# Performance work log

Hardware: AMD Instinct MI355X
Metric: run time of the kernel (lower is better)

The kernel has to match this reference:

```python
import jax, jax.numpy as jnp
import numpy as np

NF, D, H, HD, NL, FF = 5, 64, 8, 8, 2, 128   # features, d_model, heads, head_dim, layers, ffn
NQ, QL, NC = 8, 3, 3                          # qubits, quantum layers, classes


def pos_encoding(S, d):
    pos = np.arange(S, dtype=np.float32)[:, None]
    div = np.exp(np.arange(0, d, 2, dtype=np.float32) * (-np.log(10000.0) / d))
    pe = np.zeros((S, d), np.float32)
    pe[:, 0::2] = np.sin(pos * div)
    pe[:, 1::2] = np.cos(pos * div)
    return jnp.asarray(pe)


def layernorm(x, g, b, eps=1e-5):
    m = x.mean(-1, keepdims=True)
    v = ((x - m) ** 2).mean(-1, keepdims=True)
    return (x - m) * jax.lax.rsqrt(v + eps) * g + b


def apply1q(psi, U, w):
    # psi: (2,)*NQ complex state; apply 2x2 gate U on wire w
    p = jnp.moveaxis(psi, w, 0)
    sh = p.shape
    p = (U @ p.reshape(2, -1)).reshape(sh)
    return jnp.moveaxis(p, 0, w)


def cnot(psi, c, t):
    p = jnp.moveaxis(psi, (c, t), (0, 1))
    sh = p.shape
    p = p.reshape(2, 2, -1)
    p = jnp.stack([p[0], p[1, ::-1]], 0).reshape(sh)  # flip target when control=1
    return jnp.moveaxis(p, (0, 1), (c, t))


def rx_mat(t):
    c, s = jnp.cos(t / 2), jnp.sin(t / 2)
    return jnp.stack([jnp.stack([c + 0j, -1j * s]), jnp.stack([-1j * s, c + 0j])]).astype(jnp.complex64)


def rot_mat(phi, th, om):
    # qml.Rot = RZ(om) RY(th) RZ(phi)
    c, s = jnp.cos(th / 2), jnp.sin(th / 2)
    return jnp.stack([
        jnp.stack([jnp.exp(-0.5j * (phi + om)) * c, -jnp.exp(0.5j * (phi - om)) * s]),
        jnp.stack([jnp.exp(-0.5j * (phi - om)) * s, jnp.exp(0.5j * (phi + om)) * c]),
    ]).astype(jnp.complex64)


def quantum_circuit(angles, weights):
    # angles: [NQ], weights: [QL, NQ, 3]. Circuit: QL x (AngleEmbedding(RX) + StronglyEntanglingLayer(range=1))
    psi = jnp.zeros((2,) * NQ, jnp.complex64).at[(0,) * NQ].set(1.0)
    for l in range(QL):
        for w in range(NQ):
            psi = apply1q(psi, rx_mat(angles[w]), w)
        for w in range(NQ):
            psi = apply1q(psi, rot_mat(weights[l, w, 0], weights[l, w, 1], weights[l, w, 2]), w)
        for w in range(NQ):
            psi = cnot(psi, w, (w + 1) % NQ)
    prob = jnp.abs(psi) ** 2
    zs = []
    for w in range(NC):  # <Z_w> = p(0_w) - p(1_w)
        marg = prob.sum(axis=tuple(i for i in range(NQ) if i != w))
        zs.append(marg[0] - marg[1])
    # von Neumann entropy of wires 0..3 (trace out wires 4..7), natural log
    mat = psi.reshape(16, 16)
    rho = mat @ mat.conj().T
    ev = jnp.clip(jnp.linalg.eigvalsh(rho), 1e-10, 1.0)
    ent = -jnp.sum(ev * jnp.log(ev))
    return jnp.stack(zs), ent


def setup_inputs() -> dict:
    key = jax.random.key(0)
    ks = jax.random.split(key, 30)
    sc = 0.02
    inp = {
        'x': jax.random.normal(ks[0], (16, 1024, NF), jnp.float32),
        'Wemb': sc * jax.random.normal(ks[1], (NF, D)), 'bemb': jnp.zeros((D,)),
        'Wq': sc * jax.random.normal(ks[2], (NL, D, D)), 'bq': jnp.zeros((NL, D)),
        'Wk': sc * jax.random.normal(ks[3], (NL, D, D)), 'bk': jnp.zeros((NL, D)),
        'Wv': sc * jax.random.normal(ks[4], (NL, D, D)), 'bv': jnp.zeros((NL, D)),
        'Wo': sc * jax.random.normal(ks[5], (NL, D, D)), 'bo': jnp.zeros((NL, D)),
        'ln1g': jnp.ones((NL, D)), 'ln1b': jnp.zeros((NL, D)),
        'ln2g': jnp.ones((NL, D)), 'ln2b': jnp.zeros((NL, D)),
        'Wf1': sc * jax.random.normal(ks[6], (NL, D, FF)), 'bf1': jnp.zeros((NL, FF)),
        'Wf2': sc * jax.random.normal(ks[7], (NL, FF, D)), 'bf2': jnp.zeros((NL, D)),
        'Wp1': sc * jax.random.normal(ks[8], (D, 32)), 'bp1': jnp.zeros((32,)),
        'Wp2': sc * jax.random.normal(ks[9], (32, NQ)), 'bp2': jnp.zeros((NQ,)),
        'qweights': jax.random.normal(ks[10], (QL, NQ, 3)),
    }
    return inp


def reference(x, Wemb, bemb, Wq, bq, Wk, bk, Wv, bv, Wo, bo, ln1g, ln1b, ln2g, ln2b,
              Wf1, bf1, Wf2, bf2, Wp1, bp1, Wp2, bp2, qweights):
    B, S, _ = x.shape
    h = x @ Wemb + bemb + pos_encoding(S, D)[None]  # aug + dropout are identity in eval
    scale = np.float32(1.0 / np.sqrt(HD))
    for l in range(NL):
        q = (h @ Wq[l] + bq[l]).reshape(B, S, H, HD).transpose(0, 2, 1, 3)
        k = (h @ Wk[l] + bk[l]).reshape(B, S, H, HD).transpose(0, 2, 1, 3)
        v = (h @ Wv[l] + bv[l]).reshape(B, S, H, HD).transpose(0, 2, 1, 3)
        att = jax.nn.softmax(jnp.einsum('bhsd,bhtd->bhst', q, k) * scale, axis=-1)
        o = jnp.einsum('bhst,bhtd->bhsd', att, v).transpose(0, 2, 1, 3).reshape(B, S, D)
        h = layernorm(h + o @ Wo[l] + bo[l], ln1g[l], ln1b[l])
        ff = jax.nn.relu(h @ Wf1[l] + bf1[l]) @ Wf2[l] + bf2[l]
        h = layernorm(h + ff, ln2g[l], ln2b[l])
    pooled = h.mean(1)
    feats = jax.nn.relu(pooled @ Wp1 + bp1) @ Wp2 + bp2
    angles = jnp.tanh(feats) * np.float32(np.pi)
    logits, ent = jax.vmap(quantum_circuit, in_axes=(0, None))(angles, qweights)
    return logits, ent
```

## Files before the change

### kernel.cpp

```cpp
#include <hip/hip_runtime.h>
#include <math.h>

#define BB 16
#define SS 1024
#define NF 5
#define DD 64
#define HH 8
#define HDIM 8
#define NLAYER 2
#define FFD 128
#define NQ 8
#define QLAY 3
#define NC 3
#define NSWEEP 5
#define BHS_TOT (BB * HH * SS)

typedef __fp16 hf2 __attribute__((ext_vector_type(2)));
__device__ inline hf2 ash2(float f) { union { float f; hf2 h; } u; u.f = f; return u.h; }

__global__ __launch_bounds__(64) void k_embed(const float* __restrict__ x,
                                              const float* __restrict__ Wemb,
                                              const float* __restrict__ bemb,
                                              float* __restrict__ h) {
    int bs = blockIdx.x;
    int s  = bs & (SS - 1);
    int d  = threadIdx.x;
    const float* xr = x + bs * NF;
    float acc = bemb[d];
#pragma unroll
    for (int f = 0; f < NF; ++f) acc += xr[f] * Wemb[f * DD + d];
    int i = d >> 1;
    float div = expf((float)(2 * i) * (-9.210340371976184f / 64.0f));
    float ang = (float)s * div;
    float pe = (d & 1) ? cosf(ang) : sinf(ang);
    h[bs * DD + d] = acc + pe;
}

__global__ __launch_bounds__(64) void k_qkv(const float* __restrict__ h,
                                            const float* __restrict__ Wq, const float* __restrict__ bq,
                                            const float* __restrict__ Wk, const float* __restrict__ bk,
                                            const float* __restrict__ Wv, const float* __restrict__ bv,
                                            hf2* __restrict__ qh, hf2* __restrict__ kvh, int l) {
    __shared__ float hrow[4][DD];
    int d   = threadIdx.x;
    int bs0 = blockIdx.x * 4;
#pragma unroll
    for (int r = 0; r < 4; ++r) hrow[r][d] = h[(bs0 + r) * DD + d];
    __syncthreads();
    const float* wq = Wq + l * DD * DD;
    const float* wk = Wk + l * DD * DD;
    const float* wv = Wv + l * DD * DD;
    float aq[4], ak[4], av[4];
    float bqv = bq[l * DD + d], bkv = bk[l * DD + d], bvv = bv[l * DD + d];
#pragma unroll
    for (int r = 0; r < 4; ++r) { aq[r] = bqv; ak[r] = bkv; av[r] = bvv; }
#pragma unroll 4
    for (int i = 0; i < DD; ++i) {
        float wqv = wq[i * DD + d], wkv = wk[i * DD + d], wvv = wv[i * DD + d];
#pragma unroll
        for (int r = 0; r < 4; ++r) {
            float hv = hrow[r][i];
            aq[r] += hv * wqv; ak[r] += hv * wkv; av[r] += hv * wvv;
        }
    }
    int hh = d >> 3, hd = d & 7;
    const float qs = 0.3535533906f;
    float aqp[4], akp[4];
#pragma unroll
    for (int r = 0; r < 4; ++r) { aqp[r] = __shfl_xor(aq[r], 1); akp[r] = __shfl_xor(ak[r], 1); }
    if ((hd & 1) == 0) {
#pragma unroll
        for (int r = 0; r < 4; ++r) {
            int bs = bs0 + r;
            int b = bs >> 10, s = bs & 1023;
            int bh = b * HH + hh;
            int bhs = (bh << 10) | s;
            qh[bhs * 4 + (hd >> 1)] = __builtin_amdgcn_cvt_pkrtz(aq[r] * qs, aqp[r] * qs);
            int tp = s >> 1, par = s & 1;
            kvh[(bh * 512 + tp) * 16 + par * 4 + (hd >> 1)] =
                __builtin_amdgcn_cvt_pkrtz(ak[r], akp[r]);
        }
    }
#pragma unroll
    for (int r = 0; r < 4; r += 2) {
        int bs = bs0 + r;
        int b = bs >> 10, s = bs & 1023;
        int bh = b * HH + hh;
        int tp = s >> 1;
        kvh[(bh * 512 + tp) * 16 + 8 + hd] = __builtin_amdgcn_cvt_pkrtz(av[r], av[r + 1]);
    }
}

__global__ __launch_bounds__(256) void k_attn(const hf2* __restrict__ qh,
                                              const float4* __restrict__ kvh4,
                                              float* __restrict__ Apart,
                                              float* __restrict__ lpart,
                                              int nch) {
    __shared__ float4 KVs[1024];
    int bh  = blockIdx.x;
    int sg  = blockIdx.y & 3;
    int ch  = blockIdx.y >> 2;
    int tid = threadIdx.x;
    int s   = sg * 256 + tid;
    int tpc = 512 / nch;
    const float4* kp = kvh4 + (size_t)(bh * 512 + ch * tpc) * 4;
    for (int i = tid; i < tpc * 4; i += 256) KVs[i] = kp[i];
    float4 qv = ((const float4*)qh)[(bh << 10) | s];
    hf2 q01 = ash2(qv.x), q23 = ash2(qv.y), q45 = ash2(qv.z), q67 = ash2(qv.w);
    hf2 one2 = __builtin_amdgcn_cvt_pkrtz(1.f, 1.f);
    float ls = 0.f;
    float A[8] = {0,0,0,0,0,0,0,0};
    __syncthreads();
#pragma unroll 2
    for (int t = 0; t < tpc; ++t) {
        float4 f0 = KVs[4*t], f1 = KVs[4*t+1], f2 = KVs[4*t+2], f3 = KVs[4*t+3];
        float sc0 = __builtin_amdgcn_fdot2(q67, ash2(f0.w),
                    __builtin_amdgcn_fdot2(q45, ash2(f0.z),
                    __builtin_amdgcn_fdot2(q23, ash2(f0.y),
                    __builtin_amdgcn_fdot2(q01, ash2(f0.x), 0.f, false), false), false), false);
        float sc1 = __builtin_amdgcn_fdot2(q67, ash2(f1.w),
                    __builtin_amdgcn_fdot2(q45, ash2(f1.z),
                    __builtin_amdgcn_fdot2(q23, ash2(f1.y),
                    __builtin_amdgcn_fdot2(q01, ash2(f1.x), 0.f, false), false), false), false);
        float p0 = __expf(sc0), p1 = __expf(sc1);
        hf2 pp = __builtin_amdgcn_cvt_pkrtz(p0, p1);
        ls   = __builtin_amdgcn_fdot2(pp, one2,       ls,   false);
        A[0] = __builtin_amdgcn_fdot2(pp, ash2(f2.x), A[0], false);
        A[1] = __builtin_amdgcn_fdot2(pp, ash2(f2.y), A[1], false);
        A[2] = __builtin_amdgcn_fdot2(pp, ash2(f2.z), A[2], false);
        A[3] = __builtin_amdgcn_fdot2(pp, ash2(f2.w), A[3], false);
        A[4] = __builtin_amdgcn_fdot2(pp, ash2(f3.x), A[4], false);
        A[5] = __builtin_amdgcn_fdot2(pp, ash2(f3.y), A[5], false);
        A[6] = __builtin_amdgcn_fdot2(pp, ash2(f3.z), A[6], false);
        A[7] = __builtin_amdgcn_fdot2(pp, ash2(f3.w), A[7], false);
    }
    int bhs = (bh << 10) | s;
    float* arow = Apart + (((size_t)ch << 17) + bhs) * 8;
    ((float4*)arow)[0] = make_float4(A[0], A[1], A[2], A[3]);
    ((float4*)arow)[1] = make_float4(A[4], A[5], A[6], A[7]);
    lpart[((size_t)ch << 17) + bhs] = ls;
}

__global__ __launch_bounds__(128) void k_mid(const float* __restrict__ Apart,
                                             const float* __restrict__ lpart,
                                             const float* __restrict__ Wo, const float* __restrict__ bo,
                                             const float* __restrict__ g1, const float* __restrict__ b1,
                                             const float* __restrict__ Wf1, const float* __restrict__ bf1,
                                             const float* __restrict__ Wf2, const float* __restrict__ bf2,
                                             const float* __restrict__ g2, const float* __restrict__ b2,
                                             float* __restrict__ h, int l, int nch) {
    __shared__ float orow[4][DD];
    __shared__ float h1s[4][DD];
    __shared__ float frow[4][FFD];
    int t    = threadIdx.x;
    int d    = t & 63;
    int half = t >> 6;
    int bs0  = blockIdx.x * 4;
    int hh = d >> 3, hd = d & 7;
    int r0 = half * 2, r1 = r0 + 1;

#pragma unroll
    for (int rr = 0; rr < 2; ++rr) {
        int r  = r0 + rr;
        int bs = bs0 + r;
        int b = bs >> 10, s = bs & 1023;
        int bhs = ((b * HH + hh) << 10) | s;
        float a = 0.f, lt = 0.f;
        for (int ch = 0; ch < nch; ++ch) {
            a  += Apart[(((size_t)ch << 17) + bhs) * 8 + hd];
            lt += lpart[((size_t)ch << 17) + bhs];
        }
        orow[r][d] = a / lt;
    }
    __syncthreads();

    {
        const float* w = Wo + l * DD * DD;
        float bias = bo[l * DD + d];
        float acc0 = bias, acc1 = bias;
#pragma unroll 4
        for (int i = 0; i < DD; ++i) {
            float wv = w[i * DD + d];
            acc0 += orow[r0][i] * wv;
            acc1 += orow[r1][i] * wv;
        }
        float gg = g1[l * DD + d], bb = b1[l * DD + d];
        float accs[2] = {acc0, acc1};
#pragma unroll
        for (int rr = 0; rr < 2; ++rr) {
            int r = r0 + rr;
            float a = accs[rr] + h[(bs0 + r) * DD + d];
            float sum = a;
            for (int off = 32; off; off >>= 1) sum += __shfl_xor(sum, off);
            float mean = sum * (1.f / 64.f);
            float dx = a - mean;
            float vs = dx * dx;
            for (int off = 32; off; off >>= 1) vs += __shfl_xor(vs, off);
            float rstd = rsqrtf(vs * (1.f / 64.f) + 1e-5f);
            h1s[r][d] = dx * rstd * gg + bb;
        }
    }
    __syncthreads();

    {
        const float* w = Wf1 + l * DD * FFD;
        float bv = bf1[l * FFD + t];
        float a0 = bv, a1 = bv, a2 = bv, a3 = bv;
#pragma unroll 4
        for (int i = 0; i < DD; ++i) {
            float wv = w[i * FFD + t];
            a0 += h1s[0][i]*wv; a1 += h1s[1][i]*wv;
            a2 += h1s[2][i]*wv; a3 += h1s[3][i]*wv;
        }
        frow[0][t] = fmaxf(a0, 0.f); frow[1][t] = fmaxf(a1, 0.f);
        frow[2][t] = fmaxf(a2, 0.f); frow[3][t] = fmaxf(a3, 0.f);
    }
    __syncthreads();

    {
        const float* w = Wf2 + l * FFD * DD;
        float bias = bf2[l * DD + d];
        float acc0 = bias, acc1 = bias;
#pragma unroll 4
        for (int i = 0; i < FFD; ++i) {
            float wv = w[i * DD + d];
            acc0 += frow[r0][i] * wv;
            acc1 += frow[r1][i] * wv;
        }
        float gg = g2[l * DD + d], bb = b2[l * DD + d];
        float accs[2] = {acc0, acc1};
#pragma unroll
        for (int rr = 0; rr < 2; ++rr) {
            int r = r0 + rr;
            float a = accs[rr] + h1s[r][d];
            float sum = a;
            for (int off = 32; off; off >>= 1) sum += __shfl_xor(sum, off);
            float mean = sum * (1.f / 64.f);
            float dx = a - mean;
            float vs = dx * dx;
            for (int off = 32; off; off >>= 1) vs += __shfl_xor(vs, off);
            float rstd = rsqrtf(vs * (1.f / 64.f) + 1e-5f);
            h[(bs0 + r) * DD + d] = dx * rstd * gg + bb;
        }
    }
}

__global__ __launch_bounds__(64) void k_pool(const float* __restrict__ h, float* __restrict__ pp) {
    int b = blockIdx.x, c = blockIdx.y, d = threadIdx.x;
    const float* hp = h + (b * SS + c * 128) * DD + d;
    float acc = 0.f;
#pragma unroll 8
    for (int s = 0; s < 128; ++s) acc += hp[s * DD];
    pp[(b * 8 + c) * DD + d] = acc;
}

__global__ __launch_bounds__(64) void k_tail(const float* __restrict__ pp,
                                             const float* __restrict__ Wp1, const float* __restrict__ bp1,
                                             const float* __restrict__ Wp2, const float* __restrict__ bp2,
                                             const float* __restrict__ qw,
                                             float* __restrict__ out) {
    __shared__ float pool_s[DD];
    __shared__ float hid[32];
    __shared__ float ang_s[NQ];
    __shared__ float2 Ps2[256];
    int b = blockIdx.x; int L = threadIdx.x;

    {
        float acc = 0.f;
#pragma unroll
        for (int c = 0; c < 8; ++c) acc += pp[(b * 8 + c) * DD + L];
        pool_s[L] = acc * (1.f / 1024.f);
    }
    __syncthreads();
    if (L < 32) {
        float a = bp1[L];
        for (int i = 0; i < DD; ++i) a += pool_s[i] * Wp1[i * 32 + L];
        hid[L] = fmaxf(a, 0.f);
    }
    __syncthreads();
    if (L < NQ) {
        float a = bp2[L];
        for (int j = 0; j < 32; ++j) a += hid[j] * Wp2[j * NQ + L];
        ang_s[L] = tanhf(a) * 3.14159265358979f;
    }
    __syncthreads();

    float ar[4], ai[4];
#pragma unroll
    for (int r = 0; r < 4; ++r) { ar[r] = 0.f; ai[r] = 0.f; }
    if (L == 0) ar[0] = 1.f;

    for (int l = 0; l < QLAY; ++l) {
#pragma unroll
        for (int w = 0; w < NQ; ++w) {
            int p = 7 - w;
            float half = 0.5f * ang_s[w];
            float c = cosf(half), s = sinf(half);
            if (p == 7) {
#pragma unroll
                for (int lo = 0; lo < 2; ++lo) {
                    int hi = lo + 2;
                    float r0=ar[lo], m0=ai[lo], r1=ar[hi], m1=ai[hi];
                    ar[lo] = c*r0 + s*m1;  ai[lo] = c*m0 - s*r1;
                    ar[hi] = c*r1 + s*m0;  ai[hi] = c*m1 - s*r0;
                }
            } else if (p == 6) {
#pragma unroll
                for (int base = 0; base < 4; base += 2) {
                    int lo = base, hi = base + 1;
                    float r0=ar[lo], m0=ai[lo], r1=ar[hi], m1=ai[hi];
                    ar[lo] = c*r0 + s*m1;  ai[lo] = c*m0 - s*r1;
                    ar[hi] = c*r1 + s*m0;  ai[hi] = c*m1 - s*r0;
                }
            } else {
                int mask = 1 << p;
#pragma unroll
                for (int r = 0; r < 4; ++r) {
                    float pre = __shfl_xor(ar[r], mask);
                    float pim = __shfl_xor(ai[r], mask);
                    float nr = c*ar[r] + s*pim;
                    float ni = c*ai[r] - s*pre;
                    ar[r] = nr; ai[r] = ni;
                }
            }
        }
#pragma unroll
        for (int w = 0; w < NQ; ++w) {
            const float* p3 = qw + (l * NQ + w) * 3;
            float phi = p3[0], th = p3[1], om = p3[2];
            float ct = cosf(0.5f * th), st = sinf(0.5f * th);
            float al = 0.5f * (phi + om), be = 0.5f * (phi - om);
            float ca = cosf(al), sa = sinf(al), cb = cosf(be), sb = sinf(be);
            float u00r =  ct * ca, u00i = -ct * sa;
            float u01r = -st * cb, u01i = -st * sb;
            float u10r =  st * cb, u10i = -st * sb;
            float u11r =  ct * ca, u11i =  ct * sa;
            int p = 7 - w;
            if (p >= 6) {
#pragma unroll
                for (int pi_ = 0; pi_ < 2; ++pi_) {
                    int lo = (p == 7) ? pi_ : pi_ * 2;
                    int hi = (p == 7) ? pi_ + 2 : pi_ * 2 + 1;
                    float r0=ar[lo], m0=ai[lo], r1=ar[hi], m1=ai[hi];
                    ar[lo] = u00r*r0 - u00i*m0 + u01r*r1 - u01i*m1;
                    ai[lo] = u00r*m0 + u00i*r0 + u01r*m1 + u01i*r1;
                    ar[hi] = u10r*r0 - u10i*m0 + u11r*r1 - u11i*m1;
                    ai[hi] = u10r*m0 + u10i*r0 + u11r*m1 + u11i*r1;
                }
            } else {
                int mask = 1 << p;
                int bit = (L >> p) & 1;
                float car = bit ? u11r : u00r, cai = bit ? u11i : u00i;
                float cpr = bit ? u10r : u01r, cpi = bit ? u10i : u01i;
#pragma unroll
                for (int r = 0; r < 4; ++r) {
                    float pre = __shfl_xor(ar[r], mask);
                    float pim = __shfl_xor(ai[r], mask);
                    float nr = car*ar[r] - cai*ai[r] + cpr*pre - cpi*pim;
                    float ni = car*ai[r] + cai*ar[r] + cpr*pim + cpi*pre;
                    ar[r] = nr; ai[r] = ni;
                }
            }
        }
        { float t0=ar[2]; ar[2]=ar[3]; ar[3]=t0; t0=ai[2]; ai[2]=ai[3]; ai[3]=t0; }
        ar[1]=__shfl_xor(ar[1],32); ai[1]=__shfl_xor(ai[1],32);
        ar[3]=__shfl_xor(ar[3],32); ai[3]=__shfl_xor(ai[3],32);
#pragma unroll
        for (int w = 2; w <= 6; ++w) {
            int pc = 7 - w, pt = 6 - w;
            int tm = 1 << pt;
            bool ctrl = (L >> pc) & 1;
#pragma unroll
            for (int r = 0; r < 4; ++r) {
                float swr = __shfl_xor(ar[r], tm);
                float swi = __shfl_xor(ai[r], tm);
                ar[r] = ctrl ? swr : ar[r];
                ai[r] = ctrl ? swi : ai[r];
            }
        }
        {
            bool ctrl = L & 1;
            float n0r = ctrl ? ar[2] : ar[0], n2r = ctrl ? ar[0] : ar[2];
            float n0i = ctrl ? ai[2] : ai[0], n2i = ctrl ? ai[0] : ai[2];
            float n1r = ctrl ? ar[3] : ar[1], n3r = ctrl ? ar[1] : ar[3];
            float n1i = ctrl ? ai[3] : ai[1], n3i = ctrl ? ai[1] : ai[3];
            ar[0]=n0r; ar[1]=n1r; ar[2]=n2r; ar[3]=n3r;
            ai[0]=n0i; ai[1]=n1i; ai[2]=n2i; ai[3]=n3i;
        }
    }

    {
        float p0 = ar[0]*ar[0]+ai[0]*ai[0];
        float p1 = ar[1]*ar[1]+ai[1]*ai[1];
        float p2 = ar[2]*ar[2]+ai[2]*ai[2];
        float p3 = ar[3]*ar[3]+ai[3]*ai[3];
        float z0 = p0 + p1 - p2 - p3;
        float z1 = p0 - p1 + p2 - p3;
        float zs = p0 + p1 + p2 + p3;
        float z2 = (L & 32) ? -zs : zs;
#pragma unroll
        for (int off = 1; off < 64; off <<= 1) {
            z0 += __shfl_xor(z0, off);
            z1 += __shfl_xor(z1, off);
            z2 += __shfl_xor(z2, off);
        }
        if (L == 0) {
            out[b * NC + 0] = z0;
            out[b * NC + 1] = z1;
            out[b * NC + 2] = z2;
        }
    }

#pragma unroll
    for (int r = 0; r < 4; ++r) Ps2[(r << 6) | L] = make_float2(ar[r], ai[r]);
    __syncthreads();
    int c   = L >> 2;
    int seg = L & 3;
    float gr[4], gi[4];
#pragma unroll
    for (int j = 0; j < 4; ++j) {
        float2 t = Ps2[(seg * 4 + j) * 16 + c];
        gr[j] = t.x; gi[j] = t.y;
    }
    float alm = 0.f;
#pragma unroll
    for (int j = 0; j < 4; ++j) alm += gr[j]*gr[j] + gi[j]*gi[j];
    alm += __shfl_xor(alm, 1);
    alm += __shfl_xor(alm, 2);

    for (int sweep = 0; sweep < NSWEEP; ++sweep) {
#pragma unroll 1
        for (int m = 1; m <= 15; ++m) {
            int xm = m << 2;
            float pgr[4], pgi[4];
#pragma unroll
            for (int j = 0; j < 4; ++j) {
                pgr[j] = __shfl_xor(gr[j], xm);
                pgi[j] = __shfl_xor(gi[j], xm);
            }
            float bep = __shfl_xor(alm, xm);
            float d = 0.f, e = 0.f;
#pragma unroll
            for (int j = 0; j < 4; ++j) {
                d += gr[j]*pgr[j] + gi[j]*pgi[j];
                e += gr[j]*pgi[j] - gi[j]*pgr[j];
            }
            d += __shfl_xor(d, 1); e += __shfl_xor(e, 1);
            d += __shfl_xor(d, 2); e += __shfl_xor(e, 2);
            float g2 = d*d + e*e;
            float cth = 1.f, sth = 0.f, cph = 1.f, sph = 0.f, gn = 0.f;
            if (g2 > 1e-26f) {
                gn = sqrtf(g2);
                float ginv = 1.f / gn;
                cph = d * ginv; sph = -e * ginv;
                float tau = (alm - bep) * (0.5f * ginv);
                float t = ((tau >= 0.f) ? 1.f : -1.f) / (fabsf(tau) + sqrtf(1.f + tau*tau));
                cth = rsqrtf(1.f + t*t);
                sth = t * cth;
            }
#pragma unroll
            for (int j = 0; j < 4; ++j) {
                float er = cph*pgr[j] - sph*pgi[j];
                float ei = cph*pgi[j] + sph*pgr[j];
                gr[j] = cth * gr[j] + sth * er;
                gi[j] = cth * gi[j] + sth * ei;
            }
            alm = cth*cth*alm + sth*sth*bep + 2.f*cth*sth*gn;
        }
    }

    float ev = fminf(fmaxf(alm, 1e-10f), 1.0f);
    float term = -ev * logf(ev);
#pragma unroll
    for (int off = 4; off < 64; off <<= 1) term += __shfl_xor(term, off);
    if (L == 0) out[BB * NC + b] = term;
}

extern "C" void kernel_launch(void* const* d_in, const int* in_sizes, int n_in,
                              void* d_out, int out_size, void* d_ws, size_t ws_size,
                              hipStream_t stream) {
    const float* x    = (const float*)d_in[0];
    const float* Wemb = (const float*)d_in[1];
    const float* bemb = (const float*)d_in[2];
    const float* Wq   = (const float*)d_in[3];
    const float* bq   = (const float*)d_in[4];
    const float* Wk   = (const float*)d_in[5];
    const float* bk   = (const float*)d_in[6];
    const float* Wv   = (const float*)d_in[7];
    const float* bv   = (const float*)d_in[8];
    const float* Wo   = (const float*)d_in[9];
    const float* bo   = (const float*)d_in[10];
    const float* ln1g = (const float*)d_in[11];
    const float* ln1b = (const float*)d_in[12];
    const float* ln2g = (const float*)d_in[13];
    const float* ln2b = (const float*)d_in[14];
    const float* Wf1  = (const float*)d_in[15];
    const float* bf1  = (const float*)d_in[16];
    const float* Wf2  = (const float*)d_in[17];
    const float* bf2  = (const float*)d_in[18];
    const float* Wp1  = (const float*)d_in[19];
    const float* bp1  = (const float*)d_in[20];
    const float* Wp2  = (const float*)d_in[21];
    const float* bp2  = (const float*)d_in[22];
    const float* qwts = (const float*)d_in[23];
    float* out = (float*)d_out;

    const size_t M = 1u << 20;
    auto needF = [&](int nch) {
        return (size_t)(4.5 * M) + (size_t)nch * M + (size_t)nch * BHS_TOT + BB * 8 * DD + 16384;
    };
    int nch = (ws_size >= needF(4) * sizeof(float)) ? 4 : 2;

    float* ws     = (float*)d_ws;
    float* h      = ws;
    hf2*   qh     = (hf2*)(ws + M);
    hf2*   kvh    = (hf2*)(ws + M + M / 2);
    float* Apart  = ws + (M * 9) / 2;
    float* lpart  = Apart + (size_t)nch * M;
    float* pp     = lpart + (size_t)nch * BHS_TOT;

    k_embed<<<BB * SS, 64, 0, stream>>>(x, Wemb, bemb, h);
    for (int l = 0; l < NLAYER; ++l) {
        k_qkv<<<BB * SS / 4, 64, 0, stream>>>(h, Wq, bq, Wk, bk, Wv, bv, qh, kvh, l);
        k_attn<<<dim3(BB * HH, 4 * nch), 256, 0, stream>>>(qh, (const float4*)kvh, Apart, lpart, nch);
        k_mid<<<BB * SS / 4, 128, 0, stream>>>(Apart, lpart, Wo, bo, ln1g, ln1b,
                                               Wf1, bf1, Wf2, bf2, ln2g, ln2b, h, l, nch);
    }
    k_pool<<<dim3(BB, 8), 64, 0, stream>>>(h, pp);
    k_tail<<<BB, 64, 0, stream>>>(pp, Wp1, bp1, Wp2, bp2, qwts, out);
}
```

Baseline: 359.0 us.

## Compute attention with MFMA f16 matrix ops and transposed V layout

Replaces the scalar fdot2 attention loop with MFMA 16x16x32 f16 instructions for both QK^T and PV, staging the exponentiated scores through per-wave LDS to reshape them into A-operand layout. K is stored per-row and V is written transposed so that MFMA B operands load directly from global memory. The split-over-key-chunks partial sums and their reduction in k_mid are removed, with normalization done inside the attention kernel. Each MFMA uses only 8 of its 32 K slots (Q/K zero-padded, V padded in N), so much of the matrix-unit work is wasted, and K/V are read from global memory every iteration instead of from LDS.

New measurement: 319.0 us. 1.13x faster.

```diff
diff --git a/kernel.cpp b/kernel.cpp
--- a/kernel.cpp
+++ b/kernel.cpp
@@ -16,6 +16,8 @@
 #define BHS_TOT (BB * HH * SS)
 
 typedef __fp16 hf2 __attribute__((ext_vector_type(2)));
+typedef __fp16 h8  __attribute__((ext_vector_type(8)));
+typedef float  f4x __attribute__((ext_vector_type(4)));
 __device__ inline hf2 ash2(float f) { union { float f; hf2 h; } u; u.f = f; return u.h; }
 
 __global__ __launch_bounds__(64) void k_embed(const float* __restrict__ x,
@@ -40,7 +42,8 @@
                                             const float* __restrict__ Wq, const float* __restrict__ bq,
                                             const float* __restrict__ Wk, const float* __restrict__ bk,
                                             const float* __restrict__ Wv, const float* __restrict__ bv,
-                                            hf2* __restrict__ qh, hf2* __restrict__ kvh, int l) {
+                                            hf2* __restrict__ qh, hf2* __restrict__ kh,
+                                            hf2* __restrict__ vt, int l) {
     __shared__ float hrow[4][DD];
     int d   = threadIdx.x;
     int bs0 = blockIdx.x * 4;
@@ -73,82 +76,97 @@
         for (int r = 0; r < 4; ++r) {
             int bs = bs0 + r;
             int b = bs >> 10, s = bs & 1023;
-            int bh = b * HH + hh;
-            int bhs = (bh << 10) | s;
+            int bhs = ((b * HH + hh) << 10) | s;
             qh[bhs * 4 + (hd >> 1)] = __builtin_amdgcn_cvt_pkrtz(aq[r] * qs, aqp[r] * qs);
-            int tp = s >> 1, par = s & 1;
-            kvh[(bh * 512 + tp) * 16 + par * 4 + (hd >> 1)] =
-                __builtin_amdgcn_cvt_pkrtz(ak[r], akp[r]);
-        }
-    }
-#pragma unroll
-    for (int r = 0; r < 4; r += 2) {
-        int bs = bs0 + r;
-        int b = bs >> 10, s = bs & 1023;
-        int bh = b * HH + hh;
-        int tp = s >> 1;
-        kvh[(bh * 512 + tp) * 16 + 8 + hd] = __builtin_amdgcn_cvt_pkrtz(av[r], av[r + 1]);
-    }
-}
-
-__global__ __launch_bounds__(256) void k_attn(const hf2* __restrict__ qh,
-                                              const float4* __restrict__ kvh4,
-                                              float* __restrict__ Apart,
-                                              float* __restrict__ lpart,
-                                              int nch) {
-    __shared__ float4 KVs[1024];
+            kh[bhs * 4 + (hd >> 1)] = __builtin_amdgcn_cvt_pkrtz(ak[r], akp[r]);
+        }
+    }
+    {
+        int b = bs0 >> 10, s0 = bs0 & 1023;
+        int vrow = (b * HH + hh) * 8 + hd;
+        hf2* vp = vt + vrow * 512 + (s0 >> 1);
+        vp[0] = __builtin_amdgcn_cvt_pkrtz(av[0], av[1]);
+        vp[1] = __builtin_amdgcn_cvt_pkrtz(av[2], av[3]);
+    }
+}
+
+__global__ __launch_bounds__(256) void k_attn(const float4* __restrict__ qh4,
+                                              const float4* __restrict__ kh4,
+                                              const float4* __restrict__ vt4,
+                                              float* __restrict__ Ao) {
+    __shared__ float Pbuf[4][16 * 36];
     int bh  = blockIdx.x;
-    int sg  = blockIdx.y & 3;
-    int ch  = blockIdx.y >> 2;
+    int sb  = blockIdx.y;
     int tid = threadIdx.x;
-    int s   = sg * 256 + tid;
-    int tpc = 512 / nch;
-    const float4* kp = kvh4 + (size_t)(bh * 512 + ch * tpc) * 4;
-    for (int i = tid; i < tpc * 4; i += 256) KVs[i] = kp[i];
-    float4 qv = ((const float4*)qh)[(bh << 10) | s];
-    hf2 q01 = ash2(qv.x), q23 = ash2(qv.y), q45 = ash2(qv.z), q67 = ash2(qv.w);
-    hf2 one2 = __builtin_amdgcn_cvt_pkrtz(1.f, 1.f);
-    float ls = 0.f;
-    float A[8] = {0,0,0,0,0,0,0,0};
-    __syncthreads();
-#pragma unroll 2
-    for (int t = 0; t < tpc; ++t) {
-        float4 f0 = KVs[4*t], f1 = KVs[4*t+1], f2 = KVs[4*t+2], f3 = KVs[4*t+3];
-        float sc0 = __builtin_amdgcn_fdot2(q67, ash2(f0.w),
-                    __builtin_amdgcn_fdot2(q45, ash2(f0.z),
-                    __builtin_amdgcn_fdot2(q23, ash2(f0.y),
-                    __builtin_amdgcn_fdot2(q01, ash2(f0.x), 0.f, false), false), false), false);
-        float sc1 = __builtin_amdgcn_fdot2(q67, ash2(f1.w),
-                    __builtin_amdgcn_fdot2(q45, ash2(f1.z),
-                    __builtin_amdgcn_fdot2(q23, ash2(f1.y),
-                    __builtin_amdgcn_fdot2(q01, ash2(f1.x), 0.f, false), false), false), false);
-        float p0 = __expf(sc0), p1 = __expf(sc1);
-        hf2 pp = __builtin_amdgcn_cvt_pkrtz(p0, p1);
-        ls   = __builtin_amdgcn_fdot2(pp, one2,       ls,   false);
-        A[0] = __builtin_amdgcn_fdot2(pp, ash2(f2.x), A[0], false);
-        A[1] = __builtin_amdgcn_fdot2(pp, ash2(f2.y), A[1], false);
-        A[2] = __builtin_amdgcn_fdot2(pp, ash2(f2.z), A[2], false);
-        A[3] = __builtin_amdgcn_fdot2(pp, ash2(f2.w), A[3], false);
-        A[4] = __builtin_amdgcn_fdot2(pp, ash2(f3.x), A[4], false);
-        A[5] = __builtin_amdgcn_fdot2(pp, ash2(f3.y), A[5], false);
-        A[6] = __builtin_amdgcn_fdot2(pp, ash2(f3.z), A[6], false);
-        A[7] = __builtin_amdgcn_fdot2(pp, ash2(f3.w), A[7], false);
-    }
-    int bhs = (bh << 10) | s;
-    float* arow = Apart + (((size_t)ch << 17) + bhs) * 8;
-    ((float4*)arow)[0] = make_float4(A[0], A[1], A[2], A[3]);
-    ((float4*)arow)[1] = make_float4(A[4], A[5], A[6], A[7]);
-    lpart[((size_t)ch << 17) + bhs] = ls;
-}
-
-__global__ __launch_bounds__(128) void k_mid(const float* __restrict__ Apart,
-                                             const float* __restrict__ lpart,
+    int wv  = tid >> 6;
+    int L   = tid & 63;
+    int m = L & 15, quad = L >> 4;
+    union U { float4 f; h8 h; };
+    h8 hz = {0,0,0,0,0,0,0,0};
+    h8 aQ = hz;
+    if (quad == 0) { U u; u.f = qh4[(bh << 10) | (sb * 64 + wv * 16 + m)]; aQ = u.h; }
+    float* Pw = Pbuf[wv];
+    f4x Oacc = {0.f, 0.f, 0.f, 0.f};
+    float ls0 = 0.f, ls1 = 0.f, ls2 = 0.f, ls3 = 0.f;
+    int rb = quad * 4;
+    for (int kc = 0; kc < 32; ++kc) {
+        h8 bk0 = hz, bk1 = hz;
+        if (quad == 0) {
+            U u0, u1;
+            u0.f = kh4[(bh << 10) | (kc * 32 + m)];
+            u1.f = kh4[(bh << 10) | (kc * 32 + 16 + m)];
+            bk0 = u0.h; bk1 = u1.h;
+        }
+        f4x S0 = {0.f,0.f,0.f,0.f}, S1 = {0.f,0.f,0.f,0.f};
+        S0 = __builtin_amdgcn_mfma_f32_16x16x32_f16(aQ, bk0, S0, 0, 0, 0);
+        S1 = __builtin_amdgcn_mfma_f32_16x16x32_f16(aQ, bk1, S1, 0, 0, 0);
+        float p00 = __expf(S0[0]), p01 = __expf(S0[1]);
+        float p02 = __expf(S0[2]), p03 = __expf(S0[3]);
+        float p10 = __expf(S1[0]), p11 = __expf(S1[1]);
+        float p12 = __expf(S1[2]), p13 = __expf(S1[3]);
+        ls0 += p00 + p10; ls1 += p01 + p11; ls2 += p02 + p12; ls3 += p03 + p13;
+        Pw[(rb+0)*36 + m]      = p00; Pw[(rb+1)*36 + m]      = p01;
+        Pw[(rb+2)*36 + m]      = p02; Pw[(rb+3)*36 + m]      = p03;
+        Pw[(rb+0)*36 + 16 + m] = p10; Pw[(rb+1)*36 + 16 + m] = p11;
+        Pw[(rb+2)*36 + 16 + m] = p12; Pw[(rb+3)*36 + 16 + m] = p13;
+        float4 pa = *(const float4*)&Pw[m * 36 + quad * 8];
+        float4 pb = *(const float4*)&Pw[m * 36 + quad * 8 + 4];
+        hf2 c0 = __builtin_amdgcn_cvt_pkrtz(pa.x, pa.y);
+        hf2 c1 = __builtin_amdgcn_cvt_pkrtz(pa.z, pa.w);
+        hf2 c2 = __builtin_amdgcn_cvt_pkrtz(pb.x, pb.y);
+        hf2 c3 = __builtin_amdgcn_cvt_pkrtz(pb.z, pb.w);
+        h8 aP;
+        aP[0] = c0[0]; aP[1] = c0[1]; aP[2] = c1[0]; aP[3] = c1[1];
+        aP[4] = c2[0]; aP[5] = c2[1]; aP[6] = c3[0]; aP[7] = c3[1];
+        h8 bV = hz;
+        if (m < 8) {
+            U uv; uv.f = vt4[((bh * 8 + m) << 7) | (kc * 4 + quad)];
+            bV = uv.h;
+        }
+        Oacc = __builtin_amdgcn_mfma_f32_16x16x32_f16(aP, bV, Oacc, 0, 0, 0);
+    }
+#pragma unroll
+    for (int off = 1; off <= 8; off <<= 1) {
+        ls0 += __shfl_xor(ls0, off); ls1 += __shfl_xor(ls1, off);
+        ls2 += __shfl_xor(ls2, off); ls3 += __shfl_xor(ls3, off);
+    }
+    if (m < 8) {
+        int srow = sb * 64 + wv * 16 + rb;
+        int base = (((bh << 10) | srow) << 3) + m;
+        Ao[base]      = Oacc[0] / ls0;
+        Ao[base + 8]  = Oacc[1] / ls1;
+        Ao[base + 16] = Oacc[2] / ls2;
+        Ao[base + 24] = Oacc[3] / ls3;
+    }
+}
+
+__global__ __launch_bounds__(128) void k_mid(const float* __restrict__ Ao,
                                              const float* __restrict__ Wo, const float* __restrict__ bo,
                                              const float* __restrict__ g1, const float* __restrict__ b1,
                                              const float* __restrict__ Wf1, const float* __restrict__ bf1,
                                              const float* __restrict__ Wf2, const float* __restrict__ bf2,
                                              const float* __restrict__ g2, const float* __restrict__ b2,
-                                             float* __restrict__ h, int l, int nch) {
+                                             float* __restrict__ h, int l) {
     __shared__ float orow[4][DD];
     __shared__ float h1s[4][DD];
     __shared__ float frow[4][FFD];
@@ -165,12 +183,7 @@
         int bs = bs0 + r;
         int b = bs >> 10, s = bs & 1023;
         int bhs = ((b * HH + hh) << 10) | s;
-        float a = 0.f, lt = 0.f;
-        for (int ch = 0; ch < nch; ++ch) {
-            a  += Apart[(((size_t)ch << 17) + bhs) * 8 + hd];
-            lt += lpart[((size_t)ch << 17) + bhs];
-        }
-        orow[r][d] = a / lt;
+        orow[r][d] = Ao[(bhs << 3) + hd];
     }
     __syncthreads();
 
@@ -506,25 +519,21 @@
     float* out = (float*)d_out;
 
     const size_t M = 1u << 20;
-    auto needF = [&](int nch) {
-        return (size_t)(4.5 * M) + (size_t)nch * M + (size_t)nch * BHS_TOT + BB * 8 * DD + 16384;
-    };
-    int nch = (ws_size >= needF(4) * sizeof(float)) ? 4 : 2;
-
-    float* ws     = (float*)d_ws;
-    float* h      = ws;
-    hf2*   qh     = (hf2*)(ws + M);
-    hf2*   kvh    = (hf2*)(ws + M + M / 2);
-    float* Apart  = ws + (M * 9) / 2;
-    float* lpart  = Apart + (size_t)nch * M;
-    float* pp     = lpart + (size_t)nch * BHS_TOT;
+    float* ws   = (float*)d_ws;
+    float* h    = ws;
+    hf2*   qh   = (hf2*)(ws + M);
+    hf2*   kh   = (hf2*)(ws + M + M / 2);
+    hf2*   vt   = (hf2*)(ws + 2 * M);
+    float* Ao   = ws + 2 * M + M / 2;
+    float* pp   = ws + 3 * M + M / 2;
 
     k_embed<<<BB * SS, 64, 0, stream>>>(x, Wemb, bemb, h);
     for (int l = 0; l < NLAYER; ++l) {
-        k_qkv<<<BB * SS / 4, 64, 0, stream>>>(h, Wq, bq, Wk, bk, Wv, bv, qh, kvh, l);
-        k_attn<<<dim3(BB * HH, 4 * nch), 256, 0, stream>>>(qh, (const float4*)kvh, Apart, lpart, nch);
-        k_mid<<<BB * SS / 4, 128, 0, stream>>>(Apart, lpart, Wo, bo, ln1g, ln1b,
-                                               Wf1, bf1, Wf2, bf2, ln2g, ln2b, h, l, nch);
+        k_qkv<<<BB * SS / 4, 64, 0, stream>>>(h, Wq, bq, Wk, bk, Wv, bv, qh, kh, vt, l);
+        k_attn<<<dim3(BB * HH, 16), 256, 0, stream>>>((const float4*)qh, (const float4*)kh,
+                                                      (const float4*)vt, Ao);
+        k_mid<<<BB * SS / 4, 128, 0, stream>>>(Ao, Wo, bo, ln1g, ln1b,
+                                               Wf1, bf1, Wf2, bf2, ln2g, ln2b, h, l);
     }
     k_pool<<<dim3(BB, 8), 64, 0, stream>>>(h, pp);
     k_tail<<<BB, 64, 0, stream>>>(pp, Wp1, bp1, Wp2, bp2, qwts, out);
```
